# Kernel optimization log

Measured on AMD Instinct MI355X. Metric: run time of the kernel, lower is better.

The kernel has to match this reference:

```python
import jax, jax.numpy as jnp
import numpy as np

B, DM, E, P, K = 8192, 512, 4, 1024, 2
F = DM * E  # fused_input_dim = 2048


def setup_inputs() -> dict:
    key = jax.random.key(0)
    ks = jax.random.split(key, 8)
    return {
        "x_mod0": jax.random.normal(ks[0], (B, DM), jnp.float32),
        "x_mod1": jax.random.normal(ks[1], (B, DM), jnp.float32),
        "x_mod2": jax.random.normal(ks[2], (B, DM), jnp.float32),
        "x_mod3": jax.random.normal(ks[3], (B, DM), jnp.float32),
        "label": jax.random.normal(ks[4], (B, P), jnp.float32),
        "Wg": jax.random.normal(ks[5], (E, F), jnp.float32) * (1.0 / np.sqrt(F)),
        "We": jax.random.normal(ks[6], (E, F, P), jnp.float32) * (1.0 / np.sqrt(F)),
        "be": jax.random.normal(ks[7], (E, P), jnp.float32) * 0.01,
        "topk": K,
    }


def reference(x_mod0, x_mod1, x_mod2, x_mod3, label, Wg, We, be, topk):
    # fused = cat(modalities, dim=1)  -> [B, F]
    fused = jnp.concatenate([x_mod0, x_mod1, x_mod2, x_mod3], axis=1)
    # gate_scores = softmax(Linear(fused))  (Linear weight is [out,in], no bias)
    gate_scores = jax.nn.softmax(fused @ Wg.T, axis=-1)  # [B, E]
    top_k_values, top_k_indices = jax.lax.top_k(gate_scores, topk)  # [B, K]
    # Dense equivalent of per-sample expert dispatch: run every expert,
    # then gather the top-k expert outputs per token and weighted-sum them.
    all_out = jnp.einsum("bf,efp->bep", fused, We) + be  # [B, E, P]
    gathered = jnp.take_along_axis(all_out, top_k_indices[:, :, None], axis=1)  # [B, K, P]
    preds = jnp.sum(gathered * top_k_values[:, :, None], axis=1)  # [B, P]
    # loss_fn = MSE against x['label']
    loss = jnp.mean((preds - label) ** 2)
    return (loss, preds)
```

## Files before the change

kernel.cpp:

```cpp
#include <hip/hip_runtime.h>
#include <stdint.h>

#define Bsz  8192
#define DMOD 512
#define NE   4
#define NP   1024
#define NF   2048
#define BM   160
#define MAXTILES 57

typedef float  f32x4  __attribute__((ext_vector_type(4)));
typedef __bf16 bf16x8 __attribute__((ext_vector_type(8)));
typedef unsigned short u16x8 __attribute__((ext_vector_type(8)));

typedef __attribute__((address_space(3))) void       lds_void;
typedef const __attribute__((address_space(1))) void glb_void;
#define GLOAD16(gp, lp) \
  __builtin_amdgcn_global_load_lds((glb_void*)(gp), (lds_void*)(lp), 16, 0, 0)

__device__ __forceinline__ unsigned short f32_bf16(float f) {
  unsigned int u = __float_as_uint(f);
  u += 0x7FFFu + ((u >> 16) & 1u);
  return (unsigned short)(u >> 16);
}

__global__ __launch_bounds__(256) void gate_fuse(
    const float* __restrict__ x0, const float* __restrict__ x1,
    const float* __restrict__ x2, const float* __restrict__ x3,
    const float* __restrict__ Wg, const float* __restrict__ We,
    float* __restrict__ gw, int* __restrict__ pair,
    unsigned short* __restrict__ fusedB, unsigned short* __restrict__ WeT)
{
  __shared__ float sred[4][4];
  __shared__ float tsh[64][65];
  const int tid = threadIdx.x;

  if ((int)blockIdx.x < Bsz) {
    const int b = blockIdx.x;
    const int f = tid * 8;
    const float* xm  = (f < 1024) ? (f < 512 ? x0 : x1) : (f < 1536 ? x2 : x3);
    const float* src = xm + (size_t)b * DMOD + (f & 511);
    float4 v0 = *(const float4*)src;
    float4 v1 = *(const float4*)(src + 4);
    u16x8 o;
    o[0] = f32_bf16(v0.x); o[1] = f32_bf16(v0.y); o[2] = f32_bf16(v0.z); o[3] = f32_bf16(v0.w);
    o[4] = f32_bf16(v1.x); o[5] = f32_bf16(v1.y); o[6] = f32_bf16(v1.z); o[7] = f32_bf16(v1.w);
    *(u16x8*)(fusedB + (size_t)b * NF + f) = o;

    float d[4];
    #pragma unroll
    for (int e = 0; e < 4; ++e) {
      const float* w = Wg + e * NF + f;
      d[e] = v0.x * w[0] + v0.y * w[1] + v0.z * w[2] + v0.w * w[3]
           + v1.x * w[4] + v1.y * w[5] + v1.z * w[6] + v1.w * w[7];
    }
    #pragma unroll
    for (int off = 32; off; off >>= 1) {
      #pragma unroll
      for (int e = 0; e < 4; ++e) d[e] += __shfl_xor(d[e], off);
    }
    if ((tid & 63) == 0) {
      #pragma unroll
      for (int e = 0; e < 4; ++e) sred[tid >> 6][e] = d[e];
    }
    __syncthreads();
    if (tid == 0) {
      float a0 = sred[0][0] + sred[1][0] + sred[2][0] + sred[3][0];
      float a1 = sred[0][1] + sred[1][1] + sred[2][1] + sred[3][1];
      float a2 = sred[0][2] + sred[1][2] + sred[2][2] + sred[3][2];
      float a3 = sred[0][3] + sred[1][3] + sred[2][3] + sred[3][3];
      float m  = fmaxf(fmaxf(a0, a1), fmaxf(a2, a3));
      float e0 = expf(a0 - m), e1 = expf(a1 - m), e2 = expf(a2 - m), e3 = expf(a3 - m);
      float inv = 1.f / (e0 + e1 + e2 + e3);
      float p0 = e0 * inv, p1 = e1 * inv, p2 = e2 * inv, p3 = e3 * inv;
      int i1 = 0; float b1 = a0;
      if (a1 > b1) { b1 = a1; i1 = 1; }
      if (a2 > b1) { b1 = a2; i1 = 2; }
      if (a3 > b1) { b1 = a3; i1 = 3; }
      int i2 = -1; float b2 = -3.4e38f;
      if (i1 != 0 && a0 > b2) { b2 = a0; i2 = 0; }
      if (i1 != 1 && a1 > b2) { b2 = a1; i2 = 1; }
      if (i1 != 2 && a2 > b2) { b2 = a2; i2 = 2; }
      if (i1 != 3 && a3 > b2) { b2 = a3; i2 = 3; }
      gw[(size_t)b * 4 + 0] = (i1 == 0 || i2 == 0) ? p0 : 0.f;
      gw[(size_t)b * 4 + 1] = (i1 == 1 || i2 == 1) ? p1 : 0.f;
      gw[(size_t)b * 4 + 2] = (i1 == 2 || i2 == 2) ? p2 : 0.f;
      gw[(size_t)b * 4 + 3] = (i1 == 3 || i2 == 3) ? p3 : 0.f;
      int lo = min(i1, i2), hi = max(i1, i2);
      pair[b] = (lo == 0) ? (hi - 1) : (lo == 1) ? (hi + 1) : 5;
    }
  } else {
    const int tb = (int)blockIdx.x - Bsz;
    const int e  = tb >> 9;
    const int rem = tb & 511;
    const int tf = (rem & 31) * 64;
    const int tp = (rem >> 5) * 64;
    const int t4 = tid * 4;
    const float* src = We + ((size_t)e * NF + tf) * NP + tp;
    #pragma unroll
    for (int i = 0; i < 4; ++i) {
      int li = i * 1024 + t4;
      int r = li >> 6, c = li & 63;
      float4 v = *(const float4*)(src + (size_t)r * NP + c);
      tsh[c][r] = v.x; tsh[c+1][r] = v.y; tsh[c+2][r] = v.z; tsh[c+3][r] = v.w;
    }
    __syncthreads();
    unsigned short* dst = WeT + ((size_t)e * NP + tp) * NF + tf;
    #pragma unroll
    for (int i = 0; i < 4; ++i) {
      int li = i * 1024 + t4;
      int r = li >> 6, c = li & 63;
      ushort4 o;
      o.x = f32_bf16(tsh[r][c]);   o.y = f32_bf16(tsh[r][c+1]);
      o.z = f32_bf16(tsh[r][c+2]); o.w = f32_bf16(tsh[r][c+3]);
      *(ushort4*)(dst + (size_t)r * NF + c) = o;
    }
  }
}

__global__ __launch_bounds__(256) void bucket_scan(
    const int* __restrict__ pair, int* __restrict__ ridx,
    int4* __restrict__ tiletab, int* __restrict__ ntiles,
    double* __restrict__ lossAcc)
{
  __shared__ int cntS[256][6];
  __shared__ int segS[8][6];
  __shared__ int baseS[6];
  const int tid = threadIdx.x;
  int c[6] = {0, 0, 0, 0, 0, 0};
  for (int i = 0; i < 32; ++i) {
    const int code = pair[tid * 32 + i];
    #pragma unroll
    for (int b = 0; b < 6; ++b) c[b] += (code == b) ? 1 : 0;
  }
  #pragma unroll
  for (int b = 0; b < 6; ++b) cntS[tid][b] = c[b];
  __syncthreads();
  if (tid < 48) {
    const int b = tid >> 3, seg = tid & 7;
    int run = 0;
    for (int i = seg * 32; i < seg * 32 + 32; ++i) {
      const int v = cntS[i][b]; cntS[i][b] = run; run += v;
    }
    segS[seg][b] = run;
  }
  __syncthreads();
  if (tid < 6) {
    int run = 0;
    #pragma unroll
    for (int s = 0; s < 8; ++s) { const int v = segS[s][tid]; segS[s][tid] = run; run += v; }
    baseS[tid] = run;
  }
  __syncthreads();
  if (tid == 0) {
    const int e1t[6] = {0, 0, 0, 1, 1, 2};
    const int e2t[6] = {1, 2, 3, 2, 3, 3};
    int base[6];
    int off = 0, nt = 0;
    for (int b = 0; b < 6; ++b) {
      base[b] = off;
      const int cb = baseS[b];
      for (int i = 0; i < cb; i += BM)
        tiletab[nt++] = make_int4(off + i, min(BM, cb - i), e1t[b], e2t[b]);
      off += cb;
    }
    *ntiles = nt;
    *lossAcc = 0.0;
    #pragma unroll
    for (int b = 0; b < 6; ++b) baseS[b] = base[b];
  }
  __syncthreads();
  int pos[6];
  #pragma unroll
  for (int b = 0; b < 6; ++b) pos[b] = baseS[b] + segS[tid >> 5][b] + cntS[tid][b];
  for (int i = 0; i < 32; ++i) {
    const int r = tid * 32 + i;
    const int code = pair[r];
    #pragma unroll
    for (int b = 0; b < 6; ++b)
      if (code == b) { ridx[pos[b]] = r; ++pos[b]; }
  }
}

__global__ __launch_bounds__(512, 4) void moe_gemm_db(
    const unsigned short* __restrict__ fusedB,
    const unsigned short* __restrict__ WeT,
    const float* __restrict__ gw,
    const float* __restrict__ be,
    const float* __restrict__ label,
    const int* __restrict__ ntilesP,
    const int4* __restrict__ tiletab,
    const int* __restrict__ ridx,
    float* __restrict__ out,
    double* __restrict__ lossAcc)
{
  const int bid  = (int)blockIdx.x;
  const int swz  = (bid & 7) * 57 + (bid >> 3);
  const int tile = swz >> 3;
  if (tile >= *ntilesP) return;
  const int pcol = (swz & 7) * 128;

  __shared__ __align__(16) unsigned short As[2][BM * 32];
  __shared__ __align__(16) unsigned short B1s[2][128 * 32];
  __shared__ __align__(16) unsigned short B2s[2][128 * 32];
  __shared__ int   ridxS[BM];
  __shared__ float gwS[BM][2];
  __shared__ float red[8];

  const int4 te     = tiletab[tile];
  const int rowbase = te.x;
  const int vcount  = te.y;
  const int e1      = te.z;
  const int e2      = te.w;

  const int tid  = threadIdx.x;
  const int l    = tid & 63;
  const int wave = tid >> 6;
  const int wr   = wave >> 2;
  const int wc   = wave & 3;
  const int lrow = l & 15;
  const int g4   = l >> 4;
  const int schA = (l & 3) ^ ((l >> 3) & 3);

  if (tid < BM) {
    const int ri = ridx[rowbase + min(tid, vcount - 1)];
    ridxS[tid]  = ri;
    gwS[tid][0] = gw[(size_t)ri * 4 + e1];
    gwS[tid][1] = gw[(size_t)ri * 4 + e2];
  }
  __syncthreads();

  const int rowA0 = ridxS[wave * 16 + (l >> 2)];
  const int rowA1 = (wave < 2) ? ridxS[(8 + wave) * 16 + (l >> 2)] : 0;

  f32x4 acc1[5][2], acc2[5][2];
  #pragma unroll
  for (int m = 0; m < 5; ++m)
    #pragma unroll
    for (int n = 0; n < 2; ++n) {
      acc1[m][n] = f32x4{0.f, 0.f, 0.f, 0.f};
      acc2[m][n] = f32x4{0.f, 0.f, 0.f, 0.f};
    }

  auto STAGE = [&](int t, int buf) {
    const int k0 = t << 5;
    const unsigned short* B1g = WeT + ((size_t)e1 * NP + pcol) * NF + k0;
    const unsigned short* B2g = WeT + ((size_t)e2 * NP + pcol) * NF + k0;
    #pragma unroll
    for (int s = 0; s < 4; ++s) {
      const int idx = wave + s * 8;
      if (idx >= 26) continue;
      if (idx < 10) {
        const int r0  = idx * 16;
        const int row = (s == 0) ? rowA0 : rowA1;
        GLOAD16(fusedB + (size_t)row * NF + k0 + schA * 8, (char*)(&As[buf][r0 * 32]));
      } else if (idx < 18) {
        const int r0 = (idx - 10) * 16;
        GLOAD16(B1g + (size_t)(r0 + (l >> 2)) * NF + schA * 8, (char*)(&B1s[buf][r0 * 32]));
      } else {
        const int r0 = (idx - 18) * 16;
        GLOAD16(B2g + (size_t)(r0 + (l >> 2)) * NF + schA * 8, (char*)(&B2s[buf][r0 * 32]));
      }
    }
  };

  auto COMPUTE = [&](int buf) {
    bf16x8 af[5], b1f[2], b2f[2];
    #pragma unroll
    for (int m = 0; m < 5; ++m) {
      const int fr = wr * 80 + m * 16 + lrow;
      const int ch = (g4 ^ ((fr >> 1) & 3)) * 8;
      af[m] = __builtin_bit_cast(bf16x8, *(const u16x8*)(&As[buf][fr * 32 + ch]));
    }
    #pragma unroll
    for (int n = 0; n < 2; ++n) {
      const int fr = wc * 32 + n * 16 + lrow;
      const int ch = (g4 ^ ((fr >> 1) & 3)) * 8;
      b1f[n] = __builtin_bit_cast(bf16x8, *(const u16x8*)(&B1s[buf][fr * 32 + ch]));
      b2f[n] = __builtin_bit_cast(bf16x8, *(const u16x8*)(&B2s[buf][fr * 32 + ch]));
    }
    #pragma unroll
    for (int m = 0; m < 5; ++m)
      #pragma unroll
      for (int n = 0; n < 2; ++n) {
        acc1[m][n] = __builtin_amdgcn_mfma_f32_16x16x32_bf16(af[m], b1f[n], acc1[m][n], 0, 0, 0);
        acc2[m][n] = __builtin_amdgcn_mfma_f32_16x16x32_bf16(af[m], b2f[n], acc2[m][n], 0, 0, 0);
      }
  };

  STAGE(0, 0);
  STAGE(1, 1);

  #pragma unroll 1
  for (int t = 0; t < 64; ++t) {
    const int buf = t & 1;
    if (t == 63)       { asm volatile("s_waitcnt vmcnt(0)" ::: "memory"); }
    else if (wave < 2) { asm volatile("s_waitcnt vmcnt(4)" ::: "memory"); }
    else               { asm volatile("s_waitcnt vmcnt(3)" ::: "memory"); }
    __builtin_amdgcn_s_barrier();
    COMPUTE(buf);
    __builtin_amdgcn_sched_barrier(0);
    __builtin_amdgcn_s_barrier();
    if (t < 62) STAGE(t + 2, buf);
  }

  float lsum = 0.f;
  #pragma unroll
  for (int m = 0; m < 5; ++m) {
    #pragma unroll
    for (int r = 0; r < 4; ++r) {
      const int lrowi = wr * 80 + m * 16 + g4 * 4 + r;
      const bool valid = lrowi < vcount;
      const int grow = ridxS[lrowi];
      const float w1 = gwS[lrowi][0];
      const float w2 = gwS[lrowi][1];
      #pragma unroll
      for (int n = 0; n < 2; ++n) {
        const int gcol = pcol + wc * 32 + n * 16 + lrow;
        float pred = w1 * (acc1[m][n][r] + be[e1 * NP + gcol])
                   + w2 * (acc2[m][n][r] + be[e2 * NP + gcol]);
        if (valid) {
          out[1 + (size_t)grow * NP + gcol] = pred;
          float d = pred - label[(size_t)grow * NP + gcol];
          lsum += d * d;
        }
      }
    }
  }
  #pragma unroll
  for (int off = 32; off; off >>= 1) lsum += __shfl_xor(lsum, off);
  if (l == 0) red[wave] = lsum;
  __syncthreads();
  if (tid == 0) {
    double s = 0.0;
    #pragma unroll
    for (int w = 0; w < 8; ++w) s += (double)red[w];
    atomicAdd(lossAcc, s);
  }
}

__global__ void finalize_kernel(const double* __restrict__ lossAcc, float* __restrict__ out) {
  out[0] = (float)(*lossAcc * (1.0 / ((double)Bsz * (double)NP)));
}

extern "C" void kernel_launch(void* const* d_in, const int* in_sizes, int n_in,
                              void* d_out, int out_size, void* d_ws, size_t ws_size,
                              hipStream_t stream) {
  const float* x0    = (const float*)d_in[0];
  const float* x1    = (const float*)d_in[1];
  const float* x2    = (const float*)d_in[2];
  const float* x3    = (const float*)d_in[3];
  const float* label = (const float*)d_in[4];
  const float* Wg    = (const float*)d_in[5];
  const float* We    = (const float*)d_in[6];
  const float* be    = (const float*)d_in[7];
  float* out = (float*)d_out;

  char* ws = (char*)d_ws;
  unsigned short* WeT    = (unsigned short*)ws;
  unsigned short* fusedB = (unsigned short*)(ws + ((size_t)16 << 20));
  float*  gw      = (float*)(ws + ((size_t)48 << 20));
  char*   misc    = ws + ((size_t)49 << 20);
  double* lossAcc = (double*)(misc + 0);
  int*    ntiles  = (int*)(misc + 64);
  int4*   tiletab = (int4*)(misc + 256);
  int*    pair    = (int*)(misc + 4096);
  int*    ridx    = (int*)(misc + 4096 + 32768);

  gate_fuse<<<dim3(Bsz + 2048), 256, 0, stream>>>(x0, x1, x2, x3, Wg, We, gw, pair, fusedB, WeT);
  bucket_scan<<<dim3(1), 256, 0, stream>>>(pair, ridx, tiletab, ntiles, lossAcc);
  moe_gemm_db<<<dim3(MAXTILES * 8), 512, 0, stream>>>(
      fusedB, WeT, gw, be, label, ntiles, tiletab, ridx, out, lossAcc);
  finalize_kernel<<<1, 1, 0, stream>>>(lossAcc, out);
}
```

Before: 139.3 us.

## Pre-scale inputs by gate weights and fold two experts into one K=4096 GEMM

The gate kernel now writes two bf16 copies of each fused row, one scaled by each selected expert's gate weight. The GEMM can then treat the two experts as a single concatenated K=4096 reduction into one accumulator set instead of two. The GEMM tile grows to 320 rows with a 64-wide K step and an 8-phase ping-pong schedule using setprio, and the bias is applied with the gate weights in the epilogue. This removes duplicate A fragment loads and halves accumulator registers per output. In exchange it doubles the activation workspace writes, rounds x*w to bf16 instead of x, and lowers occupancy to 2 blocks.

```diff
diff --git a/kernel.cpp b/kernel.cpp
--- a/kernel.cpp
+++ b/kernel.cpp
@@ -6,8 +6,9 @@
 #define NE   4
 #define NP   1024
 #define NF   2048
-#define BM   160
-#define MAXTILES 57
+#define BM   320
+#define BN   128
+#define MAXTILES 31
 
 typedef float  f32x4  __attribute__((ext_vector_type(4)));
 typedef __bf16 bf16x8 __attribute__((ext_vector_type(8)));
@@ -24,15 +25,16 @@
   return (unsigned short)(u >> 16);
 }
 
-__global__ __launch_bounds__(256) void gate_fuse(
+__global__ __launch_bounds__(256) void gate_scale_tr(
     const float* __restrict__ x0, const float* __restrict__ x1,
     const float* __restrict__ x2, const float* __restrict__ x3,
     const float* __restrict__ Wg, const float* __restrict__ We,
     float* __restrict__ gw, int* __restrict__ pair,
-    unsigned short* __restrict__ fusedB, unsigned short* __restrict__ WeT)
+    unsigned short* __restrict__ Ap, unsigned short* __restrict__ WeT)
 {
   __shared__ float sred[4][4];
   __shared__ float tsh[64][65];
+  __shared__ float wsh[2];
   const int tid = threadIdx.x;
 
   if ((int)blockIdx.x < Bsz) {
@@ -42,10 +44,6 @@
     const float* src = xm + (size_t)b * DMOD + (f & 511);
     float4 v0 = *(const float4*)src;
     float4 v1 = *(const float4*)(src + 4);
-    u16x8 o;
-    o[0] = f32_bf16(v0.x); o[1] = f32_bf16(v0.y); o[2] = f32_bf16(v0.z); o[3] = f32_bf16(v0.w);
-    o[4] = f32_bf16(v1.x); o[5] = f32_bf16(v1.y); o[6] = f32_bf16(v1.z); o[7] = f32_bf16(v1.w);
-    *(u16x8*)(fusedB + (size_t)b * NF + f) = o;
 
     float d[4];
     #pragma unroll
@@ -88,7 +86,20 @@
       gw[(size_t)b * 4 + 3] = (i1 == 3 || i2 == 3) ? p3 : 0.f;
       int lo = min(i1, i2), hi = max(i1, i2);
       pair[b] = (lo == 0) ? (hi - 1) : (lo == 1) ? (hi + 1) : 5;
-    }
+      wsh[0] = (lo == 0) ? p0 : (lo == 1) ? p1 : p2;
+      wsh[1] = (hi == 1) ? p1 : (hi == 2) ? p2 : p3;
+    }
+    __syncthreads();
+    const float w1 = wsh[0], w2 = wsh[1];
+    float v[8] = {v0.x, v0.y, v0.z, v0.w, v1.x, v1.y, v1.z, v1.w};
+    u16x8 o1, o2;
+    #pragma unroll
+    for (int j = 0; j < 8; ++j) {
+      o1[j] = f32_bf16(v[j] * w1);
+      o2[j] = f32_bf16(v[j] * w2);
+    }
+    *(u16x8*)(Ap + (size_t)b * NF + f) = o1;
+    *(u16x8*)(Ap + ((size_t)Bsz + b) * NF + f) = o2;
   } else {
     const int tb = (int)blockIdx.x - Bsz;
     const int e  = tb >> 9;
@@ -182,8 +193,8 @@
   }
 }
 
-__global__ __launch_bounds__(512, 4) void moe_gemm_db(
-    const unsigned short* __restrict__ fusedB,
+__global__ __launch_bounds__(512, 2) void moe_gemm_8p(
+    const unsigned short* __restrict__ Ap,
     const unsigned short* __restrict__ WeT,
     const float* __restrict__ gw,
     const float* __restrict__ be,
@@ -195,14 +206,13 @@
     double* __restrict__ lossAcc)
 {
   const int bid  = (int)blockIdx.x;
-  const int swz  = (bid & 7) * 57 + (bid >> 3);
+  const int swz  = (bid & 7) * MAXTILES + (bid >> 3);
   const int tile = swz >> 3;
   if (tile >= *ntilesP) return;
-  const int pcol = (swz & 7) * 128;
-
-  __shared__ __align__(16) unsigned short As[2][BM * 32];
-  __shared__ __align__(16) unsigned short B1s[2][128 * 32];
-  __shared__ __align__(16) unsigned short B2s[2][128 * 32];
+  const int pcol = (swz & 7) * BN;
+
+  __shared__ __align__(16) unsigned short As[2][BM * 64];
+  __shared__ __align__(16) unsigned short Bs[2][BN * 64];
   __shared__ int   ridxS[BM];
   __shared__ float gwS[BM][2];
   __shared__ float red[8];
@@ -220,7 +230,8 @@
   const int wc   = wave & 3;
   const int lrow = l & 15;
   const int g4   = l >> 4;
-  const int schA = (l & 3) ^ ((l >> 3) & 3);
+  const int lr8  = l >> 3;
+  const int schA = (l & 7) ^ lr8;
 
   if (tid < BM) {
     const int ri = ridx[rowbase + min(tid, vcount - 1)];
@@ -230,86 +241,119 @@
   }
   __syncthreads();
 
-  const int rowA0 = ridxS[wave * 16 + (l >> 2)];
-  const int rowA1 = (wave < 2) ? ridxS[(8 + wave) * 16 + (l >> 2)] : 0;
-
-  f32x4 acc1[5][2], acc2[5][2];
-  #pragma unroll
-  for (int m = 0; m < 5; ++m)
-    #pragma unroll
-    for (int n = 0; n < 2; ++n) {
-      acc1[m][n] = f32x4{0.f, 0.f, 0.f, 0.f};
-      acc2[m][n] = f32x4{0.f, 0.f, 0.f, 0.f};
-    }
-
-  auto STAGE = [&](int t, int buf) {
-    const int k0 = t << 5;
-    const unsigned short* B1g = WeT + ((size_t)e1 * NP + pcol) * NF + k0;
-    const unsigned short* B2g = WeT + ((size_t)e2 * NP + pcol) * NF + k0;
-    #pragma unroll
-    for (int s = 0; s < 4; ++s) {
-      const int idx = wave + s * 8;
-      if (idx >= 26) continue;
-      if (idx < 10) {
-        const int r0  = idx * 16;
-        const int row = (s == 0) ? rowA0 : rowA1;
-        GLOAD16(fusedB + (size_t)row * NF + k0 + schA * 8, (char*)(&As[buf][r0 * 32]));
-      } else if (idx < 18) {
-        const int r0 = (idx - 10) * 16;
-        GLOAD16(B1g + (size_t)(r0 + (l >> 2)) * NF + schA * 8, (char*)(&B1s[buf][r0 * 32]));
-      } else {
-        const int r0 = (idx - 18) * 16;
-        GLOAD16(B2g + (size_t)(r0 + (l >> 2)) * NF + schA * 8, (char*)(&B2s[buf][r0 * 32]));
-      }
-    }
+  int rA[5];
+  #pragma unroll
+  for (int s = 0; s < 5; ++s) rA[s] = ridxS[wave * 8 + s * 64 + lr8];
+
+  f32x4 acc[10][2];
+  #pragma unroll
+  for (int m = 0; m < 10; ++m)
+    #pragma unroll
+    for (int n = 0; n < 2; ++n) acc[m][n] = f32x4{0.f, 0.f, 0.f, 0.f};
+
+  auto STAGE_A = [&](int t1, unsigned short* Ad, int s) {
+    const int k0 = (t1 & 31) << 6;
+    const unsigned short* Ag = Ap + (size_t)(t1 >> 5) * ((size_t)Bsz * NF);
+    GLOAD16(Ag + (size_t)rA[s] * NF + k0 + schA * 8, (char*)(Ad + (wave + s * 8) * 512));
   };
-
-  auto COMPUTE = [&](int buf) {
-    bf16x8 af[5], b1f[2], b2f[2];
-    #pragma unroll
-    for (int m = 0; m < 5; ++m) {
-      const int fr = wr * 80 + m * 16 + lrow;
-      const int ch = (g4 ^ ((fr >> 1) & 3)) * 8;
-      af[m] = __builtin_bit_cast(bf16x8, *(const u16x8*)(&As[buf][fr * 32 + ch]));
-    }
+  auto STAGE_B = [&](int t1, unsigned short* Bd, int s) {
+    const int k0 = (t1 & 31) << 6;
+    const unsigned short* Bg =
+        WeT + ((size_t)((t1 >> 5) ? e2 : e1) * NP + pcol) * NF + k0;
+    const int idx = wave + s * 8;
+    GLOAD16(Bg + (size_t)(idx * 8 + lr8) * NF + schA * 8, (char*)(Bd + idx * 512));
+  };
+
+  auto LDA = [&](bf16x8 (&af)[5], const unsigned short* Ar, int mbase, int ks) {
+    #pragma unroll
+    for (int i = 0; i < 5; ++i) {
+      const int fr = wr * 160 + (mbase + i) * 16 + lrow;
+      const int ch = ((g4 + ks * 4) ^ (fr & 7)) * 8;
+      af[i] = __builtin_bit_cast(bf16x8, *(const u16x8*)(Ar + fr * 64 + ch));
+    }
+  };
+  auto LDB = [&](bf16x8 (&bfr)[2], const unsigned short* Br, int ks) {
     #pragma unroll
     for (int n = 0; n < 2; ++n) {
       const int fr = wc * 32 + n * 16 + lrow;
-      const int ch = (g4 ^ ((fr >> 1) & 3)) * 8;
-      b1f[n] = __builtin_bit_cast(bf16x8, *(const u16x8*)(&B1s[buf][fr * 32 + ch]));
-      b2f[n] = __builtin_bit_cast(bf16x8, *(const u16x8*)(&B2s[buf][fr * 32 + ch]));
-    }
-    #pragma unroll
-    for (int m = 0; m < 5; ++m)
+      const int ch = ((g4 + ks * 4) ^ (fr & 7)) * 8;
+      bfr[n] = __builtin_bit_cast(bf16x8, *(const u16x8*)(Br + fr * 64 + ch));
+    }
+  };
+  auto MM = [&](bf16x8 (&af)[5], bf16x8 (&bfr)[2], int mbase) {
+    #pragma unroll
+    for (int i = 0; i < 5; ++i)
       #pragma unroll
-      for (int n = 0; n < 2; ++n) {
-        acc1[m][n] = __builtin_amdgcn_mfma_f32_16x16x32_bf16(af[m], b1f[n], acc1[m][n], 0, 0, 0);
-        acc2[m][n] = __builtin_amdgcn_mfma_f32_16x16x32_bf16(af[m], b2f[n], acc2[m][n], 0, 0, 0);
-      }
+      for (int n = 0; n < 2; ++n)
+        acc[mbase + i][n] =
+            __builtin_amdgcn_mfma_f32_16x16x32_bf16(af[i], bfr[n], acc[mbase + i][n], 0, 0, 0);
   };
 
-  STAGE(0, 0);
-  STAGE(1, 1);
+  #pragma unroll
+  for (int s = 0; s < 5; ++s) STAGE_A(0, As[0], s);
+  STAGE_B(0, Bs[0], 0);
+  STAGE_B(0, Bs[0], 1);
+  asm volatile("s_waitcnt vmcnt(0)" ::: "memory");
+  __builtin_amdgcn_s_barrier();
 
   #pragma unroll 1
   for (int t = 0; t < 64; ++t) {
-    const int buf = t & 1;
-    if (t == 63)       { asm volatile("s_waitcnt vmcnt(0)" ::: "memory"); }
-    else if (wave < 2) { asm volatile("s_waitcnt vmcnt(4)" ::: "memory"); }
-    else               { asm volatile("s_waitcnt vmcnt(3)" ::: "memory"); }
-    __builtin_amdgcn_s_barrier();
-    COMPUTE(buf);
+    unsigned short* Ar = As[t & 1];
+    unsigned short* Br = Bs[t & 1];
+    unsigned short* Aw = As[(t + 1) & 1];
+    unsigned short* Bw = Bs[(t + 1) & 1];
+    const bool st = (t < 63);
+    bf16x8 af[5], bf0[2], bf1[2];
+
+    LDA(af, Ar, 0, 0);
+    LDB(bf0, Br, 0);
+    if (st) { STAGE_A(t + 1, Aw, 0); STAGE_A(t + 1, Aw, 1); STAGE_A(t + 1, Aw, 2); }
+    __builtin_amdgcn_s_barrier();
+    asm volatile("s_waitcnt lgkmcnt(0)" ::: "memory");
     __builtin_amdgcn_sched_barrier(0);
-    __builtin_amdgcn_s_barrier();
-    if (t < 62) STAGE(t + 2, buf);
+    __builtin_amdgcn_s_setprio(1);
+    MM(af, bf0, 0);
+    __builtin_amdgcn_s_setprio(0);
+    __builtin_amdgcn_s_barrier();
+
+    LDA(af, Ar, 5, 0);
+    if (st) { STAGE_A(t + 1, Aw, 3); STAGE_A(t + 1, Aw, 4); }
+    __builtin_amdgcn_s_barrier();
+    asm volatile("s_waitcnt lgkmcnt(0)" ::: "memory");
+    __builtin_amdgcn_sched_barrier(0);
+    __builtin_amdgcn_s_setprio(1);
+    MM(af, bf0, 5);
+    __builtin_amdgcn_s_setprio(0);
+    __builtin_amdgcn_s_barrier();
+
+    LDA(af, Ar, 0, 1);
+    LDB(bf1, Br, 1);
+    if (st) { STAGE_B(t + 1, Bw, 0); STAGE_B(t + 1, Bw, 1); }
+    __builtin_amdgcn_s_barrier();
+    asm volatile("s_waitcnt lgkmcnt(0)" ::: "memory");
+    __builtin_amdgcn_sched_barrier(0);
+    __builtin_amdgcn_s_setprio(1);
+    MM(af, bf1, 0);
+    __builtin_amdgcn_s_setprio(0);
+    __builtin_amdgcn_s_barrier();
+
+    LDA(af, Ar, 5, 1);
+    __builtin_amdgcn_s_barrier();
+    asm volatile("s_waitcnt lgkmcnt(0)" ::: "memory");
+    __builtin_amdgcn_sched_barrier(0);
+    __builtin_amdgcn_s_setprio(1);
+    MM(af, bf1, 5);
+    __builtin_amdgcn_s_setprio(0);
+    asm volatile("s_waitcnt vmcnt(0)" ::: "memory");
+    __builtin_amdgcn_s_barrier();
   }
 
   float lsum = 0.f;
   #pragma unroll
-  for (int m = 0; m < 5; ++m) {
+  for (int m = 0; m < 10; ++m) {
     #pragma unroll
     for (int r = 0; r < 4; ++r) {
-      const int lrowi = wr * 80 + m * 16 + g4 * 4 + r;
+      const int lrowi = wr * 160 + m * 16 + g4 * 4 + r;
       const bool valid = lrowi < vcount;
       const int grow = ridxS[lrowi];
       const float w1 = gwS[lrowi][0];
@@ -317,8 +361,7 @@
       #pragma unroll
       for (int n = 0; n < 2; ++n) {
         const int gcol = pcol + wc * 32 + n * 16 + lrow;
-        float pred = w1 * (acc1[m][n][r] + be[e1 * NP + gcol])
-                   + w2 * (acc2[m][n][r] + be[e2 * NP + gcol]);
+        float pred = acc[m][n][r] + w1 * be[e1 * NP + gcol] + w2 * be[e2 * NP + gcol];
         if (valid) {
           out[1 + (size_t)grow * NP + gcol] = pred;
           float d = pred - label[(size_t)grow * NP + gcol];
@@ -357,19 +400,19 @@
   float* out = (float*)d_out;
 
   char* ws = (char*)d_ws;
-  unsigned short* WeT    = (unsigned short*)ws;
-  unsigned short* fusedB = (unsigned short*)(ws + ((size_t)16 << 20));
-  float*  gw      = (float*)(ws + ((size_t)48 << 20));
-  char*   misc    = ws + ((size_t)49 << 20);
+  unsigned short* WeT = (unsigned short*)ws;
+  unsigned short* Ap  = (unsigned short*)(ws + ((size_t)16 << 20));
+  char*   misc    = ws + ((size_t)80 << 20);
   double* lossAcc = (double*)(misc + 0);
   int*    ntiles  = (int*)(misc + 64);
   int4*   tiletab = (int4*)(misc + 256);
   int*    pair    = (int*)(misc + 4096);
   int*    ridx    = (int*)(misc + 4096 + 32768);
-
-  gate_fuse<<<dim3(Bsz + 2048), 256, 0, stream>>>(x0, x1, x2, x3, Wg, We, gw, pair, fusedB, WeT);
+  float*  gw      = (float*)(misc + 4096 + 65536);
+
+  gate_scale_tr<<<dim3(Bsz + 2048), 256, 0, stream>>>(x0, x1, x2, x3, Wg, We, gw, pair, Ap, WeT);
   bucket_scan<<<dim3(1), 256, 0, stream>>>(pair, ridx, tiletab, ntiles, lossAcc);
-  moe_gemm_db<<<dim3(MAXTILES * 8), 512, 0, stream>>>(
-      fusedB, WeT, gw, be, label, ntiles, tiletab, ridx, out, lossAcc);
+  moe_gemm_8p<<<dim3(MAXTILES * 8), 512, 0, stream>>>(
+      Ap, WeT, gw, be, label, ntiles, tiletab, ridx, out, lossAcc);
   finalize_kernel<<<1, 1, 0, stream>>>(lossAcc, out);
 }
```

Result: slower. 180.0 us (+29.2%).
